# Kernel tuning notes

Hardware: AMD Instinct MI355X
Metric: run time of the kernel (lower is better)

Reference implementation:

```python
import jax, jax.numpy as jnp
import numpy as np

N = 100000      # nodes
E = 1600000     # edges (avg degree 16)
F_IN = 128
H1, H2, C = 200, 50, 10


def _lin(key, fin, fout):
    # Glorot-uniform-ish init
    lim = (6.0 / (fin + fout)) ** 0.5
    return jax.random.uniform(key, (fin, fout), jnp.float32, -lim, lim)


def setup_inputs() -> dict:
    key = jax.random.key(0)
    ks = jax.random.split(key, 11)
    x = jax.random.normal(ks[0], (N, F_IN), jnp.float32)
    edge_index = jax.random.randint(ks[1], (2, E), 0, N, jnp.int32)
    return {
        "x": x,
        "edge_index": edge_index,
        "W_l1": _lin(ks[2], F_IN, H1), "b1": jnp.zeros((H1,), jnp.float32), "W_r1": _lin(ks[3], F_IN, H1),
        "W_l2": _lin(ks[4], H1, H2),   "b2": jnp.zeros((H2,), jnp.float32), "W_r2": _lin(ks[5], H1, H2),
        "W_l3": _lin(ks[6], H2, C),    "b3": jnp.zeros((C,), jnp.float32),  "W_r3": _lin(ks[7], H2, C),
    }


def _sage_conv_max(x, src, dst, W_l, b, W_r):
    # gather neighbor (source) features, scatter-max into destination nodes
    agg = jax.ops.segment_max(x[src], dst, num_segments=N)   # [N, F]
    agg = jnp.where(jnp.isfinite(agg), agg, 0.0)             # empty segments -> 0 (PyG behavior)
    return agg @ W_l + b + x @ W_r


def reference(x, edge_index, W_l1, b1, W_r1, W_l2, b2, W_r2, W_l3, b3, W_r3):
    src, dst = edge_index[0], edge_index[1]
    h = _sage_conv_max(x, src, dst, W_l1, b1, W_r1)   # [N, 200]
    h = _sage_conv_max(h, src, dst, W_l2, b2, W_r2)   # [N, 50]
    h = _sage_conv_max(h, src, dst, W_l3, b3, W_r3)   # [N, 10]
    return jax.nn.log_softmax(h, axis=1)
```

## Files before the change

### kernel.cpp

```cpp
#include <hip/hip_runtime.h>
#include <cstdint>
#include <cstddef>

#define N_NODES 100000
#define N_EDGES 1600000
#define F_IN    128
#define H1D     200
#define H2D     50
#define NCLS    10

#define P1 256
#define P2 416
#define P3 128
#define H2OFF 56
#define X1PD 48
#define X2PD 80

#define BSH 9
#define BMASK 511
#define NB 196
#define EPB 8192

typedef __attribute__((ext_vector_type(8))) short short8;
typedef __attribute__((ext_vector_type(4))) float f32x4;

__device__ __forceinline__ unsigned short f2b(float f) {
    union { float f; uint32_t u; } v; v.f = f;
    uint32_t u = v.u;
    return (unsigned short)((u + 0x7fffu + ((u >> 16) & 1u)) >> 16);
}
__device__ __forceinline__ float b2f(unsigned short b) {
    union { uint32_t u; float f; } v; v.u = ((uint32_t)b) << 16;
    return v.f;
}
__device__ __forceinline__ void upk(uint32_t p, float& a, float& b) {
    union { uint32_t u; float f; } lo, hi;
    lo.u = (p & 0xffffu) << 16;
    hi.u = p & 0xffff0000u;
    a = lo.f; b = hi.f;
}

__device__ __forceinline__ uint32_t b2s12(unsigned short h) {
    int e = (int)(h & 0x7FFF) - 15488;
    e = e < 0 ? 0 : (e > 2047 ? 2047 : e);
    return (h & 0x8000) ? (uint32_t)(2047 - e) : (uint32_t)(2048 + e);
}
__device__ __forceinline__ unsigned short s122b(uint32_t t) {
    if (t >= 2048u) { uint32_t mag = t - 2048u; return mag ? (unsigned short)(mag + 15488u) : (unsigned short)0; }
    uint32_t mag = 2047u - t;   return mag ? (unsigned short)(0x8000u | (mag + 15488u)) : (unsigned short)0;
}
__device__ __forceinline__ void pack12(const uint32_t* t, uint32_t& d0, uint32_t& d1, uint32_t& d2) {
    d0 = t[0] | (t[1] << 12) | (t[2] << 24);
    d1 = (t[2] >> 8) | (t[3] << 4) | (t[4] << 16) | (t[5] << 28);
    d2 = (t[5] >> 4) | (t[6] << 8) | (t[7] << 20);
}

__device__ __forceinline__ int block_excl_scan_256(int v, int* wsum) {
    const int tid = threadIdx.x;
    const int lane = tid & 63;
    const int wid = tid >> 6;
    int incl = v;
    #pragma unroll
    for (int off = 1; off < 64; off <<= 1) {
        int t = __shfl_up(incl, off, 64);
        if (lane >= off) incl += t;
    }
    if (lane == 63) wsum[wid] = incl;
    __syncthreads();
    if (tid == 0) {
        int s = 0;
        #pragma unroll
        for (int k = 0; k < 4; k++) { int t = wsum[k]; wsum[k] = s; s += t; }
    }
    __syncthreads();
    return wsum[wid] + incl - v;
}

__global__ __launch_bounds__(256) void csr_p0(const int* __restrict__ dst,
                                              int* __restrict__ bcnt, int E) {
    __shared__ int c[256];
    const int tid = threadIdx.x;
    c[tid] = 0;
    __syncthreads();
    const int base = blockIdx.x * EPB;
    #pragma unroll 4
    for (int i = 0; i < EPB / 256; i++) {
        int e = base + i * 256 + tid;
        if (e < E) atomicAdd(&c[dst[e] >> BSH], 1);
    }
    __syncthreads();
    int v = c[tid];
    if (v > 0) atomicAdd(&bcnt[tid], v);
}

__global__ __launch_bounds__(256) void csr_bscan(const int* __restrict__ bcnt,
                                                 int* __restrict__ g_bbase,
                                                 int* __restrict__ g_bcur) {
    __shared__ int wsum[4];
    const int tid = threadIdx.x;
    int v = (tid < NB) ? bcnt[tid] : 0;
    int excl = block_excl_scan_256(v, wsum);
    if (tid < NB) { g_bbase[tid] = excl; g_bcur[tid] = excl; }
    if (tid == NB) g_bbase[NB] = excl;
}

__global__ __launch_bounds__(256) void csr_p1(const int* __restrict__ src,
                                              const int* __restrict__ dst,
                                              int* __restrict__ g_bcur,
                                              uint32_t* __restrict__ staging, int E) {
    __shared__ int cnt[256];
    __shared__ int base_s[256];
    const int tid = threadIdx.x;
    const int base = blockIdx.x * EPB;
    cnt[tid] = 0;
    __syncthreads();
    #pragma unroll 4
    for (int i = 0; i < EPB / 256; i++) {
        int e = base + i * 256 + tid;
        if (e < E) atomicAdd(&cnt[dst[e] >> BSH], 1);
    }
    __syncthreads();
    int v = cnt[tid];
    if (v > 0) base_s[tid] = atomicAdd(&g_bcur[tid], v);
    cnt[tid] = 0;
    __syncthreads();
    #pragma unroll 4
    for (int i = 0; i < EPB / 256; i++) {
        int e = base + i * 256 + tid;
        if (e < E) {
            int d = dst[e], s = src[e];
            int b = d >> BSH;
            int r = atomicAdd(&cnt[b], 1);
            staging[base_s[b] + r] = ((uint32_t)s << BSH) | (uint32_t)(d & BMASK);
        }
    }
}

__global__ __launch_bounds__(256) void csr_p2(const uint32_t* __restrict__ staging,
                                              const int* __restrict__ g_bbase,
                                              int* __restrict__ row_ptr,
                                              int* __restrict__ col_src, int N, int E) {
    __shared__ int cnt[512];
    __shared__ int wsum[4];
    const int tid = threadIdx.x;
    const int nodeBase = blockIdx.x << BSH;
    cnt[tid] = 0; cnt[tid + 256] = 0;
    __syncthreads();
    const int lo = g_bbase[blockIdx.x];
    const int hi = g_bbase[blockIdx.x + 1];
    for (int j = lo + tid; j < hi; j += 256)
        atomicAdd(&cnt[staging[j] & BMASK], 1);
    __syncthreads();
    int v0 = cnt[2 * tid], v1 = cnt[2 * tid + 1];
    int pexcl = block_excl_scan_256(v0 + v1, wsum);
    __syncthreads();
    cnt[2 * tid]     = lo + pexcl;
    cnt[2 * tid + 1] = lo + pexcl + v0;
    int node0 = nodeBase + 2 * tid;
    if (node0 < N)     row_ptr[node0]     = lo + pexcl;
    if (node0 + 1 < N) row_ptr[node0 + 1] = lo + pexcl + v0;
    __syncthreads();
    for (int j = lo + tid; j < hi; j += 256) {
        uint32_t rec = staging[j];
        int p = atomicAdd(&cnt[rec & BMASK], 1);
        col_src[p] = (int)(rec >> BSH);
    }
    if (blockIdx.x == 0 && tid == 0) row_ptr[N] = E;
}

__global__ void build_bt_kernel(const float* __restrict__ Wl, const float* __restrict__ Wr,
                                unsigned short* __restrict__ Bt,
                                int K1, int k2off, int K2, int M, int P) {
    int idx = blockIdx.x * blockDim.x + threadIdx.x;
    if (idx >= M * P) return;
    int m = idx / P, k = idx - m * P;
    float v = 0.0f;
    if (k < K1)                          v = Wl[(size_t)k * M + m];
    else if (k >= k2off && k < k2off+K2) v = Wr[(size_t)(k - k2off) * M + m];
    Bt[(size_t)m * P + k] = f2b(v);
}

__global__ void conv_x_kernel(const float* __restrict__ x,
                              unsigned short* __restrict__ A1,
                              uint32_t* __restrict__ X12, int N) {
    int idx = blockIdx.x * blockDim.x + threadIdx.x;
    if (idx >= N * 16) return;
    int row = idx >> 4, g = idx & 15;
    const float* xp = x + (size_t)row * F_IN + g * 8;
    unsigned short h[8];
    #pragma unroll
    for (int i = 0; i < 8; i++) h[i] = f2b(xp[i]);
    ushort4 o0 = {h[0], h[1], h[2], h[3]};
    ushort4 o1 = {h[4], h[5], h[6], h[7]};
    *(ushort4*)(A1 + (size_t)row * P1 + F_IN + g * 8) = o0;
    *(ushort4*)(A1 + (size_t)row * P1 + F_IN + g * 8 + 4) = o1;
    uint32_t t[8];
    #pragma unroll
    for (int i = 0; i < 8; i++) t[i] = b2s12(h[i]);
    uint32_t d0, d1, d2;
    pack12(t, d0, d1, d2);
    uint32_t* op = X12 + (size_t)row * X1PD + g * 3;
    op[0] = d0; op[1] = d1; op[2] = d2;
}

__global__ void pack12_h1_kernel(const unsigned short* __restrict__ A2,
                                 uint32_t* __restrict__ X12, int N) {
    int idx = blockIdx.x * blockDim.x + threadIdx.x;
    if (idx >= N * 25) return;
    int row = idx / 25, g = idx - row * 25;
    ushort4 h0 = *(const ushort4*)(A2 + (size_t)row * P2 + H1D + g * 8);
    ushort4 h1 = *(const ushort4*)(A2 + (size_t)row * P2 + H1D + g * 8 + 4);
    uint32_t t[8] = {b2s12(h0.x), b2s12(h0.y), b2s12(h0.z), b2s12(h0.w),
                     b2s12(h1.x), b2s12(h1.y), b2s12(h1.z), b2s12(h1.w)};
    uint32_t d0, d1, d2;
    pack12(t, d0, d1, d2);
    uint32_t* op = X12 + (size_t)row * X2PD + g * 3;
    op[0] = d0; op[1] = d1; op[2] = d2;
}

__global__ void pad_zero_kernel(unsigned short* __restrict__ A, int pitch,
                                int begin, int width, int N) {
    int idx = blockIdx.x * blockDim.x + threadIdx.x;
    if (idx >= N * width) return;
    int r = idx / width, c = idx - r * width;
    A[(size_t)r * pitch + begin + c] = 0;
}

template <int F, int G, int PITCHD>
__global__ __launch_bounds__(256) void agg_max_12(
    const uint32_t* __restrict__ X12,
    const int* __restrict__ row_ptr, const int* __restrict__ col_src,
    unsigned short* __restrict__ O, int opitch, int N) {
    static_assert(G == 16 || G == 32, "G must be 16/32");
    const int wave = (blockIdx.x * blockDim.x + threadIdx.x) >> 6;
    const int lane = threadIdx.x & 63;
    if (wave >= N) return;
    const int beg = row_ptr[wave];
    const int end = row_ptr[wave + 1];
    constexpr int LOG2G = (G == 16) ? 4 : 5;
    constexpr int EPW = 64 / G;
    const int l = lane & (G - 1);
    const int grp = lane >> LOG2G;
    const int f0 = l * 8;
    const bool act = (f0 < F);

    uint32_t t[8];
    #pragma unroll
    for (int i = 0; i < 8; i++) t[i] = 0u;

    auto mrg = [&](uint32_t d0, uint32_t d1, uint32_t d2) {
        uint32_t v;
        v = d0 & 0xFFFu;                        t[0] = t[0] > v ? t[0] : v;
        v = (d0 >> 12) & 0xFFFu;                t[1] = t[1] > v ? t[1] : v;
        v = (d0 >> 24) | ((d1 & 0xFu) << 8);    t[2] = t[2] > v ? t[2] : v;
        v = (d1 >> 4) & 0xFFFu;                 t[3] = t[3] > v ? t[3] : v;
        v = (d1 >> 16) & 0xFFFu;                t[4] = t[4] > v ? t[4] : v;
        v = (d1 >> 28) | ((d2 & 0xFFu) << 4);   t[5] = t[5] > v ? t[5] : v;
        v = (d2 >> 8) & 0xFFFu;                 t[6] = t[6] > v ? t[6] : v;
        v = d2 >> 20;                           t[7] = t[7] > v ? t[7] : v;
    };

    int j = beg + grp;
    for (; j + EPW < end; j += 2 * EPW) {
        int s0 = col_src[j];
        int s1 = col_src[j + EPW];
        uint32_t a0 = 0, a1 = 0, a2 = 0, b0 = 0, b1 = 0, b2 = 0;
        if (act) {
            const uint32_t* p0 = X12 + (size_t)s0 * PITCHD + l * 3;
            const uint32_t* p1 = X12 + (size_t)s1 * PITCHD + l * 3;
            a0 = p0[0]; a1 = p0[1]; a2 = p0[2];
            b0 = p1[0]; b1 = p1[1]; b2 = p1[2];
        }
        mrg(a0, a1, a2);
        mrg(b0, b1, b2);
    }
    if (j < end && act) {
        const uint32_t* p = X12 + (size_t)col_src[j] * PITCHD + l * 3;
        mrg(p[0], p[1], p[2]);
    }

    #pragma unroll
    for (int off = G; off < 64; off <<= 1) {
        #pragma unroll
        for (int i = 0; i < 8; i++) {
            uint32_t v = (uint32_t)__shfl_xor((int)t[i], off, 64);
            t[i] = t[i] > v ? t[i] : v;
        }
    }

    if (grp == 0 && act) {
        unsigned short* op = O + (size_t)wave * opitch;
        uint4 o = {0u, 0u, 0u, 0u};
        if (beg != end) {
            unsigned short h[8];
            #pragma unroll
            for (int i = 0; i < 8; i++) h[i] = s122b(t[i]);
            o.x = (uint32_t)h[0] | ((uint32_t)h[1] << 16);
            o.y = (uint32_t)h[2] | ((uint32_t)h[3] << 16);
            o.z = (uint32_t)h[4] | ((uint32_t)h[5] << 16);
            o.w = (uint32_t)h[6] | ((uint32_t)h[7] << 16);
        }
        *(uint4*)(op + f0) = o;
    }
}

template <int F, int G>
__global__ __launch_bounds__(256) void agg_max_v3(
    const unsigned short* __restrict__ X, int xpitch,
    const int* __restrict__ row_ptr, const int* __restrict__ col_src,
    unsigned short* __restrict__ O, int opitch, int N) {
    static_assert(G == 8 || G == 16 || G == 32, "G must be 8/16/32");
    static_assert(G * 8 >= F, "group must cover F");
    const int wave = (blockIdx.x * blockDim.x + threadIdx.x) >> 6;
    const int lane = threadIdx.x & 63;
    if (wave >= N) return;
    const int beg = row_ptr[wave];
    const int end = row_ptr[wave + 1];
    constexpr int LOG2G = (G == 8) ? 3 : ((G == 16) ? 4 : 5);
    constexpr int EPW = 64 / G;
    const int l = lane & (G - 1);
    const int grp = lane >> LOG2G;
    const int f0 = l * 8;
    const bool act = (f0 < F);

    float m[8];
    #pragma unroll
    for (int i = 0; i < 8; i++) m[i] = -INFINITY;

    auto ld = [&](int s) -> uint4 {
        if (act) return *(const uint4*)(X + (size_t)s * xpitch + f0);
        return (uint4){0u, 0u, 0u, 0u};
    };
    auto mrg = [&](const uint4& v) {
        if (act) {
            float a, b;
            upk(v.x, a, b); m[0] = fmaxf(m[0], a); m[1] = fmaxf(m[1], b);
            upk(v.y, a, b); m[2] = fmaxf(m[2], a); m[3] = fmaxf(m[3], b);
            upk(v.z, a, b); m[4] = fmaxf(m[4], a); m[5] = fmaxf(m[5], b);
            upk(v.w, a, b); m[6] = fmaxf(m[6], a); m[7] = fmaxf(m[7], b);
        }
    };

    int j = beg + grp;
    for (; j + EPW < end; j += 2 * EPW) {
        int s0 = col_src[j];
        int s1 = col_src[j + EPW];
        uint4 v0 = ld(s0), v1 = ld(s1);
        mrg(v0); mrg(v1);
    }
    if (j < end) mrg(ld(col_src[j]));

    #pragma unroll
    for (int off = G; off < 64; off <<= 1) {
        #pragma unroll
        for (int i = 0; i < 8; i++)
            m[i] = fmaxf(m[i], __shfl_xor(m[i], off, 64));
    }

    if (grp == 0 && act) {
        unsigned short* op = O + (size_t)wave * opitch;
        const bool empty = (beg == end);
        if (f0 + 8 <= F) {
            uint4 o = {0u, 0u, 0u, 0u};
            if (!empty) {
                o.x = (uint32_t)f2b(m[0]) | ((uint32_t)f2b(m[1]) << 16);
                o.y = (uint32_t)f2b(m[2]) | ((uint32_t)f2b(m[3]) << 16);
                o.z = (uint32_t)f2b(m[4]) | ((uint32_t)f2b(m[5]) << 16);
                o.w = (uint32_t)f2b(m[6]) | ((uint32_t)f2b(m[7]) << 16);
            }
            *(uint4*)(op + f0) = o;
        } else {
            for (int i = 0; f0 + i < F; i++)
                op[f0 + i] = empty ? (unsigned short)0 : f2b(m[i]);
        }
    }
}

template <int NCT, bool LSM>
__global__ __launch_bounds__(256) void gemm_mfma_v2(
    const unsigned short* __restrict__ A, int P,
    const unsigned short* __restrict__ Bt,
    const float* __restrict__ bias,
    float* __restrict__ Cf,
    unsigned short* __restrict__ Cb, int cbPitch, int cbOff,
    int Nrows, int M) {
    __shared__ short As[64 * 40];
    __shared__ short Bs[NCT * 16 * 40];
    const int tid = threadIdx.x;
    const int wv = tid >> 6;
    const int lane = tid & 63;
    const int q = lane >> 4;
    const int mi = lane & 15;
    const int rowBase = blockIdx.x * 64;

    f32x4 acc[NCT];
    #pragma unroll
    for (int c = 0; c < NCT; c++) acc[c] = (f32x4){0.f, 0.f, 0.f, 0.f};

    const int srow = tid >> 2;
    const int sseg = tid & 3;
    const int grow = rowBase + srow;
    constexpr int BSLOTS = NCT * 64;
    constexpr int BITERS = (BSLOTS + 255) / 256;

    for (int kt = 0; kt < P; kt += 32) {
        uint4 va = {0u, 0u, 0u, 0u};
        if (grow < Nrows) va = *(const uint4*)(A + (size_t)grow * P + kt + sseg * 8);
        *(uint4*)(&As[srow * 40 + sseg * 8]) = va;
        #pragma unroll
        for (int i = 0; i < BITERS; i++) {
            int slot = i * 256 + tid;
            if (slot < BSLOTS) {
                int br = slot >> 2;
                int bs = slot & 3;
                uint4 vb = {0u, 0u, 0u, 0u};
                if (br < M) vb = *(const uint4*)(Bt + (size_t)br * P + kt + bs * 8);
                *(uint4*)(&Bs[br * 40 + bs * 8]) = vb;
            }
        }
        __syncthreads();
        short8 a = *(const short8*)(&As[(wv * 16 + mi) * 40 + q * 8]);
        #pragma unroll
        for (int c = 0; c < NCT; c++) {
            short8 b = *(const short8*)(&Bs[(c * 16 + mi) * 40 + q * 8]);
            acc[c] = __builtin_amdgcn_mfma_f32_16x16x32_bf16(a, b, acc[c], 0, 0, 0);
        }
        __syncthreads();
    }

    if (LSM) {
        float bv = (mi < M) ? bias[mi] : 0.0f;
        #pragma unroll
        for (int r = 0; r < 4; r++) {
            float v = acc[0][r] + bv;
            float mx = (mi < M) ? v : -INFINITY;
            #pragma unroll
            for (int off = 1; off < 16; off <<= 1)
                mx = fmaxf(mx, __shfl_xor(mx, off, 64));
            float ex = (mi < M) ? expf(v - mx) : 0.0f;
            float sm = ex;
            #pragma unroll
            for (int off = 1; off < 16; off <<= 1)
                sm += __shfl_xor(sm, off, 64);
            int row = rowBase + wv * 16 + q * 4 + r;
            if (mi < M && row < Nrows)
                Cf[(size_t)row * M + mi] = v - mx - logf(sm);
        }
    } else {
        #pragma unroll
        for (int c = 0; c < NCT; c++) {
            int col = c * 16 + mi;
            if (col >= M) continue;
            float bv = bias[col];
            #pragma unroll
            for (int r = 0; r < 4; r++) {
                int row = rowBase + wv * 16 + q * 4 + r;
                if (row >= Nrows) continue;
                float v = acc[c][r] + bv;
                if (Cf) Cf[(size_t)row * M + col] = v;
                else    Cb[(size_t)row * cbPitch + cbOff + col] = f2b(v);
            }
        }
    }
}

extern "C" void kernel_launch(void* const* d_in, const int* in_sizes, int n_in,
                              void* d_out, int out_size, void* d_ws, size_t ws_size,
                              hipStream_t stream) {
    const float* x    = (const float*)d_in[0];
    const int*   eidx = (const int*)d_in[1];
    const float* Wl1  = (const float*)d_in[2];
    const float* b1   = (const float*)d_in[3];
    const float* Wr1  = (const float*)d_in[4];
    const float* Wl2  = (const float*)d_in[5];
    const float* b2   = (const float*)d_in[6];
    const float* Wr2  = (const float*)d_in[7];
    const float* Wl3  = (const float*)d_in[8];
    const float* b3   = (const float*)d_in[9];
    const float* Wr3  = (const float*)d_in[10];
    const int* srcp = eidx;
    const int* dstp = eidx + N_EDGES;
    float* out = (float*)d_out;
    (void)ws_size; (void)in_sizes; (void)n_in; (void)out_size;

    char* w = (char*)d_ws;
    size_t off = 0;
    auto alloc = [&](size_t bytes) -> char* {
        char* p = w + off;
        off += (bytes + 255) & ~(size_t)255;
        return p;
    };
    int* bcnt     = (int*)alloc(sizeof(int) * 256);
    int* g_bbase  = (int*)alloc(sizeof(int) * 256);
    int* g_bcur   = (int*)alloc(sizeof(int) * 256);
    int* row_ptr  = (int*)alloc(sizeof(int) * (N_NODES + 1));
    int* col_src  = (int*)alloc(sizeof(int) * N_EDGES);
    uint32_t* staging = (uint32_t*)alloc(sizeof(uint32_t) * N_EDGES);
    unsigned short* A1  = (unsigned short*)alloc(sizeof(short) * (size_t)N_NODES * P1);
    unsigned short* A2  = (unsigned short*)alloc(sizeof(short) * (size_t)N_NODES * P2);
    unsigned short* A3  = (unsigned short*)alloc(sizeof(short) * (size_t)N_NODES * P3);
    uint32_t* X12_1 = (uint32_t*)alloc(sizeof(uint32_t) * (size_t)N_NODES * X1PD);
    unsigned short* Bt1 = (unsigned short*)alloc(sizeof(short) * H1D * P1);
    unsigned short* Bt2 = (unsigned short*)alloc(sizeof(short) * H2D * P2);
    unsigned short* Bt3 = (unsigned short*)alloc(sizeof(short) * NCLS * P3);
    uint32_t* X12_2 = (uint32_t*)A1;

    const int EDGE_BLKS = (N_EDGES + EPB - 1) / EPB;
    hipMemsetAsync(bcnt, 0, sizeof(int) * 256, stream);
    csr_p0<<<EDGE_BLKS, 256, 0, stream>>>(dstp, bcnt, N_EDGES);
    csr_bscan<<<1, 256, 0, stream>>>(bcnt, g_bbase, g_bcur);
    csr_p1<<<EDGE_BLKS, 256, 0, stream>>>(srcp, dstp, g_bcur, staging, N_EDGES);
    csr_p2<<<NB, 256, 0, stream>>>(staging, g_bbase, row_ptr, col_src, N_NODES, N_EDGES);

    build_bt_kernel<<<(H1D * P1 + 255) / 256, 256, 0, stream>>>(Wl1, Wr1, Bt1, F_IN, F_IN, F_IN, H1D, P1);
    build_bt_kernel<<<(H2D * P2 + 255) / 256, 256, 0, stream>>>(Wl2, Wr2, Bt2, H1D, H1D, H1D, H2D, P2);
    build_bt_kernel<<<(NCLS * P3 + 255) / 256, 256, 0, stream>>>(Wl3, Wr3, Bt3, H2D, H2OFF, H2D, NCLS, P3);
    conv_x_kernel<<<(N_NODES * 16 + 255) / 256, 256, 0, stream>>>(x, A1, X12_1, N_NODES);
    pad_zero_kernel<<<(N_NODES * 16 + 255) / 256, 256, 0, stream>>>(A2, P2, 2 * H1D, P2 - 2 * H1D, N_NODES);
    pad_zero_kernel<<<(N_NODES * 6 + 255) / 256, 256, 0, stream>>>(A3, P3, H2D, H2OFF - H2D, N_NODES);
    pad_zero_kernel<<<(N_NODES * 22 + 255) / 256, 256, 0, stream>>>(A3, P3, H2OFF + H2D, P3 - H2OFF - H2D, N_NODES);

    const int aggBlocks = (N_NODES + 3) / 4;
    const int rowTiles = (N_NODES + 63) / 64;

    agg_max_12<F_IN, 16, X1PD><<<aggBlocks, 256, 0, stream>>>(X12_1, row_ptr, col_src, A1, P1, N_NODES);
    gemm_mfma_v2<13, false><<<rowTiles, 256, 0, stream>>>(A1, P1, Bt1, b1, nullptr, A2, P2, H1D, N_NODES, H1D);

    pack12_h1_kernel<<<(N_NODES * 25 + 255) / 256, 256, 0, stream>>>(A2, X12_2, N_NODES);

    agg_max_12<H1D, 32, X2PD><<<aggBlocks, 256, 0, stream>>>(X12_2, row_ptr, col_src, A2, P2, N_NODES);
    gemm_mfma_v2<4, false><<<rowTiles, 256, 0, stream>>>(A2, P2, Bt2, b2, nullptr, A3, P3, H2OFF, N_NODES, H2D);

    agg_max_v3<H2D, 8><<<aggBlocks, 256, 0, stream>>>(A3 + H2OFF, P3, row_ptr, col_src, A3, P3, N_NODES);
    gemm_mfma_v2<1, true><<<rowTiles, 256, 0, stream>>>(A3, P3, Bt3, b3, out, nullptr, 0, 0, N_NODES, NCLS);
}
```

Measured before the change: 510.9 us.

## Fuse 12-bit packing and padding into GEMM epilogues and merge setup kernels

The layer-1 GEMM epilogue now stages its bf16 output in shared memory and writes the 12-bit packed gather table directly, which removes the separate pack kernel. It also zeroes the A2 padding columns, so the pad_zero launches are dropped. The layer-2 GEMM additionally writes a compact 64-pitch bf16 table that the layer-3 aggregation gathers from, which should give denser gathers than the strided A3 reads. The three weight-transpose kernels are merged into one launch, and the workspace buffers are aliased to shrink the footprint. The cost is larger shared memory in the layer-1 GEMM, which may lower its occupancy.

```diff
diff --git a/kernel.cpp b/kernel.cpp
--- a/kernel.cpp
+++ b/kernel.cpp
@@ -168,16 +168,35 @@
     if (blockIdx.x == 0 && tid == 0) row_ptr[N] = E;
 }
 
-__global__ void build_bt_kernel(const float* __restrict__ Wl, const float* __restrict__ Wr,
-                                unsigned short* __restrict__ Bt,
-                                int K1, int k2off, int K2, int M, int P) {
+__global__ void build_bt_all(const float* __restrict__ Wl1, const float* __restrict__ Wr1,
+                             const float* __restrict__ Wl2, const float* __restrict__ Wr2,
+                             const float* __restrict__ Wl3, const float* __restrict__ Wr3,
+                             unsigned short* __restrict__ Bt1,
+                             unsigned short* __restrict__ Bt2,
+                             unsigned short* __restrict__ Bt3) {
+    constexpr int S1 = H1D * P1, S2 = H2D * P2, S3 = NCLS * P3;
     int idx = blockIdx.x * blockDim.x + threadIdx.x;
-    if (idx >= M * P) return;
-    int m = idx / P, k = idx - m * P;
-    float v = 0.0f;
-    if (k < K1)                          v = Wl[(size_t)k * M + m];
-    else if (k >= k2off && k < k2off+K2) v = Wr[(size_t)(k - k2off) * M + m];
-    Bt[(size_t)m * P + k] = f2b(v);
+    if (idx < S1) {
+        int m = idx / P1, k = idx - m * P1;
+        float v = 0.0f;
+        if (k < F_IN)            v = Wl1[(size_t)k * H1D + m];
+        else if (k < 2 * F_IN)   v = Wr1[(size_t)(k - F_IN) * H1D + m];
+        Bt1[idx] = f2b(v);
+    } else if (idx < S1 + S2) {
+        int j = idx - S1;
+        int m = j / P2, k = j - m * P2;
+        float v = 0.0f;
+        if (k < H1D)             v = Wl2[(size_t)k * H2D + m];
+        else if (k < 2 * H1D)    v = Wr2[(size_t)(k - H1D) * H2D + m];
+        Bt2[j] = f2b(v);
+    } else if (idx < S1 + S2 + S3) {
+        int j = idx - S1 - S2;
+        int m = j / P3, k = j - m * P3;
+        float v = 0.0f;
+        if (k < H2D)                          v = Wl3[(size_t)k * NCLS + m];
+        else if (k >= H2OFF && k < H2OFF+H2D) v = Wr3[(size_t)(k - H2OFF) * NCLS + m];
+        Bt3[j] = f2b(v);
+    }
 }
 
 __global__ void conv_x_kernel(const float* __restrict__ x,
@@ -203,27 +222,12 @@
     op[0] = d0; op[1] = d1; op[2] = d2;
 }
 
-__global__ void pack12_h1_kernel(const unsigned short* __restrict__ A2,
-                                 uint32_t* __restrict__ X12, int N) {
+__global__ void pad_a3_kernel(unsigned short* __restrict__ A3, int N) {
     int idx = blockIdx.x * blockDim.x + threadIdx.x;
-    if (idx >= N * 25) return;
-    int row = idx / 25, g = idx - row * 25;
-    ushort4 h0 = *(const ushort4*)(A2 + (size_t)row * P2 + H1D + g * 8);
-    ushort4 h1 = *(const ushort4*)(A2 + (size_t)row * P2 + H1D + g * 8 + 4);
-    uint32_t t[8] = {b2s12(h0.x), b2s12(h0.y), b2s12(h0.z), b2s12(h0.w),
-                     b2s12(h1.x), b2s12(h1.y), b2s12(h1.z), b2s12(h1.w)};
-    uint32_t d0, d1, d2;
-    pack12(t, d0, d1, d2);
-    uint32_t* op = X12 + (size_t)row * X2PD + g * 3;
-    op[0] = d0; op[1] = d1; op[2] = d2;
-}
-
-__global__ void pad_zero_kernel(unsigned short* __restrict__ A, int pitch,
-                                int begin, int width, int N) {
-    int idx = blockIdx.x * blockDim.x + threadIdx.x;
-    if (idx >= N * width) return;
-    int r = idx / width, c = idx - r * width;
-    A[(size_t)r * pitch + begin + c] = 0;
+    if (idx >= N * 28) return;
+    int r = idx / 28, c = idx - r * 28;
+    int col = (c < 6) ? (50 + c) : (100 + c);
+    A3[(size_t)r * P3 + col] = 0;
 }
 
 template <int F, int G, int PITCHD>
@@ -376,16 +380,22 @@
     }
 }
 
-template <int NCT, bool LSM>
-__global__ __launch_bounds__(256) void gemm_mfma_v2(
+template <int NCT, int MODE>
+__global__ __launch_bounds__(256) void gemm_mfma_v3(
     const unsigned short* __restrict__ A, int P,
     const unsigned short* __restrict__ Bt,
     const float* __restrict__ bias,
     float* __restrict__ Cf,
     unsigned short* __restrict__ Cb, int cbPitch, int cbOff,
+    uint32_t* __restrict__ X12out,
+    unsigned short* __restrict__ Htab,
     int Nrows, int M) {
-    __shared__ short As[64 * 40];
-    __shared__ short Bs[NCT * 16 * 40];
+    constexpr int ABSZ = 2560 + NCT * 640;
+    constexpr int SSZ = (MODE == 1) ? (ABSZ > 12800 ? ABSZ : 12800) : ABSZ;
+    __shared__ short smem[SSZ];
+    short* As = smem;
+    short* Bs = smem + 2560;
+    short* Hs = smem;
     const int tid = threadIdx.x;
     const int wv = tid >> 6;
     const int lane = tid & 63;
@@ -428,7 +438,7 @@
         __syncthreads();
     }
 
-    if (LSM) {
+    if constexpr (MODE == 3) {
         float bv = (mi < M) ? bias[mi] : 0.0f;
         #pragma unroll
         for (int r = 0; r < 4; r++) {
@@ -457,8 +467,33 @@
                 int row = rowBase + wv * 16 + q * 4 + r;
                 if (row >= Nrows) continue;
                 float v = acc[c][r] + bv;
-                if (Cf) Cf[(size_t)row * M + col] = v;
-                else    Cb[(size_t)row * cbPitch + cbOff + col] = f2b(v);
+                unsigned short h = f2b(v);
+                Cb[(size_t)row * cbPitch + cbOff + col] = h;
+                if constexpr (MODE == 1)
+                    Hs[(wv * 16 + q * 4 + r) * 200 + col] = (short)h;
+                if constexpr (MODE == 2)
+                    if (col < H2D) Htab[(size_t)row * 64 + col] = h;
+            }
+        }
+        if constexpr (MODE == 1) {
+            for (int k = tid; k < 64 * 16; k += 256) {
+                int r = k >> 4, c = k & 15;
+                int row = rowBase + r;
+                if (row < Nrows) Cb[(size_t)row * cbPitch + 2 * H1D + c] = 0;
+            }
+            __syncthreads();
+            for (int k = tid; k < 64 * 25; k += 256) {
+                int r = k / 25, g = k - r * 25;
+                int row = rowBase + r;
+                if (row >= Nrows) continue;
+                const short* hp = &Hs[r * 200 + g * 8];
+                uint32_t t[8];
+                #pragma unroll
+                for (int i = 0; i < 8; i++) t[i] = b2s12((unsigned short)hp[i]);
+                uint32_t d0, d1, d2;
+                pack12(t, d0, d1, d2);
+                uint32_t* op = X12out + (size_t)row * X2PD + g * 3;
+                op[0] = d0; op[1] = d1; op[2] = d2;
             }
         }
     }
@@ -495,15 +530,17 @@
     int* g_bcur   = (int*)alloc(sizeof(int) * 256);
     int* row_ptr  = (int*)alloc(sizeof(int) * (N_NODES + 1));
     int* col_src  = (int*)alloc(sizeof(int) * N_EDGES);
-    uint32_t* staging = (uint32_t*)alloc(sizeof(uint32_t) * N_EDGES);
+    char* Z = alloc(32u * 1024 * 1024);
+    uint32_t* staging = (uint32_t*)Z;
+    uint32_t* X12_1   = (uint32_t*)(Z + 8u * 1024 * 1024);
+    uint32_t* X12_2   = (uint32_t*)Z;
     unsigned short* A1  = (unsigned short*)alloc(sizeof(short) * (size_t)N_NODES * P1);
     unsigned short* A2  = (unsigned short*)alloc(sizeof(short) * (size_t)N_NODES * P2);
     unsigned short* A3  = (unsigned short*)alloc(sizeof(short) * (size_t)N_NODES * P3);
-    uint32_t* X12_1 = (uint32_t*)alloc(sizeof(uint32_t) * (size_t)N_NODES * X1PD);
     unsigned short* Bt1 = (unsigned short*)alloc(sizeof(short) * H1D * P1);
     unsigned short* Bt2 = (unsigned short*)alloc(sizeof(short) * H2D * P2);
     unsigned short* Bt3 = (unsigned short*)alloc(sizeof(short) * NCLS * P3);
-    uint32_t* X12_2 = (uint32_t*)A1;
+    unsigned short* X16_3 = A1;
 
     const int EDGE_BLKS = (N_EDGES + EPB - 1) / EPB;
     hipMemsetAsync(bcnt, 0, sizeof(int) * 256, stream);
@@ -512,25 +549,20 @@
     csr_p1<<<EDGE_BLKS, 256, 0, stream>>>(srcp, dstp, g_bcur, staging, N_EDGES);
     csr_p2<<<NB, 256, 0, stream>>>(staging, g_bbase, row_ptr, col_src, N_NODES, N_EDGES);
 
-    build_bt_kernel<<<(H1D * P1 + 255) / 256, 256, 0, stream>>>(Wl1, Wr1, Bt1, F_IN, F_IN, F_IN, H1D, P1);
-    build_bt_kernel<<<(H2D * P2 + 255) / 256, 256, 0, stream>>>(Wl2, Wr2, Bt2, H1D, H1D, H1D, H2D, P2);
-    build_bt_kernel<<<(NCLS * P3 + 255) / 256, 256, 0, stream>>>(Wl3, Wr3, Bt3, H2D, H2OFF, H2D, NCLS, P3);
+    constexpr int BT_TOTAL = H1D * P1 + H2D * P2 + NCLS * P3;
+    build_bt_all<<<(BT_TOTAL + 255) / 256, 256, 0, stream>>>(Wl1, Wr1, Wl2, Wr2, Wl3, Wr3, Bt1, Bt2, Bt3);
     conv_x_kernel<<<(N_NODES * 16 + 255) / 256, 256, 0, stream>>>(x, A1, X12_1, N_NODES);
-    pad_zero_kernel<<<(N_NODES * 16 + 255) / 256, 256, 0, stream>>>(A2, P2, 2 * H1D, P2 - 2 * H1D, N_NODES);
-    pad_zero_kernel<<<(N_NODES * 6 + 255) / 256, 256, 0, stream>>>(A3, P3, H2D, H2OFF - H2D, N_NODES);
-    pad_zero_kernel<<<(N_NODES * 22 + 255) / 256, 256, 0, stream>>>(A3, P3, H2OFF + H2D, P3 - H2OFF - H2D, N_NODES);
+    pad_a3_kernel<<<(N_NODES * 28 + 255) / 256, 256, 0, stream>>>(A3, N_NODES);
 
     const int aggBlocks = (N_NODES + 3) / 4;
     const int rowTiles = (N_NODES + 63) / 64;
 
     agg_max_12<F_IN, 16, X1PD><<<aggBlocks, 256, 0, stream>>>(X12_1, row_ptr, col_src, A1, P1, N_NODES);
-    gemm_mfma_v2<13, false><<<rowTiles, 256, 0, stream>>>(A1, P1, Bt1, b1, nullptr, A2, P2, H1D, N_NODES, H1D);
-
-    pack12_h1_kernel<<<(N_NODES * 25 + 255) / 256, 256, 0, stream>>>(A2, X12_2, N_NODES);
+    gemm_mfma_v3<13, 1><<<rowTiles, 256, 0, stream>>>(A1, P1, Bt1, b1, nullptr, A2, P2, H1D, X12_2, nullptr, N_NODES, H1D);
 
     agg_max_12<H1D, 32, X2PD><<<aggBlocks, 256, 0, stream>>>(X12_2, row_ptr, col_src, A2, P2, N_NODES);
-    gemm_mfma_v2<4, false><<<rowTiles, 256, 0, stream>>>(A2, P2, Bt2, b2, nullptr, A3, P3, H2OFF, N_NODES, H2D);
-
-    agg_max_v3<H2D, 8><<<aggBlocks, 256, 0, stream>>>(A3 + H2OFF, P3, row_ptr, col_src, A3, P3, N_NODES);
-    gemm_mfma_v2<1, true><<<rowTiles, 256, 0, stream>>>(A3, P3, Bt3, b3, out, nullptr, 0, 0, N_NODES, NCLS);
-}
+    gemm_mfma_v3<4, 2><<<rowTiles, 256, 0, stream>>>(A2, P2, Bt2, b2, nullptr, A3, P3, H2OFF, nullptr, X16_3, N_NODES, H2D);
+
+    agg_max_v3<H2D, 8><<<aggBlocks, 256, 0, stream>>>(X16_3, 64, row_ptr, col_src, A3, P3, N_NODES);
+    gemm_mfma_v3<1, 3><<<rowTiles, 256, 0, stream>>>(A3, P3, Bt3, b3, out, nullptr, 0, 0, nullptr, nullptr, N_NODES, NCLS);
+}
```

Result: faster. 487.9 us (-4.5%).
